# Kernel tuning notes

Measured on AMD Instinct MI355X. Metric: run time of the kernel, lower is better.

Reference implementation:

```python
import jax, jax.numpy as jnp
import numpy as np
import math

B, T, EMB = 4, 2048, 1024
PAD_TAIL = 256  # last keys marked as padding


def setup_inputs() -> dict:
    key = jax.random.key(0)
    kq, kk, kv = jax.random.split(key, 3)
    query = jax.random.normal(kq, (B, T, EMB), dtype=jnp.float32)
    k = jax.random.normal(kk, (B, T, EMB), dtype=jnp.float32)
    value = jax.random.normal(kv, (B, T, EMB), dtype=jnp.float32)
    # padding mask: 1 = valid, 0 = padded (last PAD_TAIL keys padded)
    attention_mask = jnp.concatenate(
        [jnp.ones((B, T - PAD_TAIL), dtype=jnp.int32),
         jnp.zeros((B, PAD_TAIL), dtype=jnp.int32)], axis=1)
    return {"query": query, "key": k, "value": value,
            "attention_mask": attention_mask}


def reference(query, key, value, attention_mask):
    Bq, Tq, emb = query.shape
    Tk = key.shape[1]
    scale = 1.0 / math.sqrt(emb)
    # [B, Tq, Tk]
    scores = jnp.einsum('bqd,bkd->bqk', query, key) * scale
    neg_inf = jnp.float32(-jnp.inf)
    if Tq == Tk:  # mask_future=True and square -> causal mask
        causal = jnp.triu(jnp.ones((Tq, Tk), dtype=bool), k=1)
        scores = jnp.where(causal[None, :, :], neg_inf, scores)
    key_pad = (attention_mask == 0)[:, None, :]  # [B, 1, Tk]
    scores = jnp.where(key_pad, neg_inf, scores)
    attn = jax.nn.softmax(scores, axis=-1)
    # attn_dropout = 0.0 -> identity
    out = jnp.einsum('bqk,bkd->bqd', attn, value)
    return out
```

## Files before the change

### kernel.cpp

```cpp
#include <hip/hip_runtime.h>
#include <stdint.h>

#define TB 2048
#define DD 1024

typedef __bf16 bf16x8 __attribute__((ext_vector_type(8)));
typedef float  f32x16 __attribute__((ext_vector_type(16)));
typedef int    int4v  __attribute__((ext_vector_type(4)));
typedef unsigned u32;

__device__ __forceinline__ u32 pack2(float hi, float lo) {
  return (__float_as_uint(hi) & 0xffff0000u) | (__float_as_uint(lo) >> 16);
}
__device__ __forceinline__ bf16x8 pack8(const float f[8]) {
  int4v w;
  w.x = (int)pack2(f[1], f[0]);
  w.y = (int)pack2(f[3], f[2]);
  w.z = (int)pack2(f[5], f[4]);
  w.w = (int)pack2(f[7], f[6]);
  return __builtin_bit_cast(bf16x8, w);
}

__global__ __launch_bounds__(256)
void conv_all(const float* __restrict__ Q, const float* __restrict__ K,
              const float* __restrict__ V,
              unsigned short* __restrict__ Qf, unsigned short* __restrict__ Kf,
              unsigned short* __restrict__ Vf) {
  __shared__ __align__(16) float t[64 * 260];
  if (blockIdx.x < 512) {
    const int isQ = blockIdx.x >> 8;
    const int bid = blockIdx.x & 255;
    const float* src0 = isQ ? Q : K;
    unsigned short* dst0 = isQ ? Qf : Kf;
    const float scl = isQ ? 0.03125f : 1.0f;
    const int b  = bid >> 6;
    const int kt = bid & 63;
    const int lt  = threadIdx.x & 63;
    const int row = lt & 31, hi = lt >> 5;
    const int wv  = threadIdx.x >> 6;
    const float* src = src0 + ((size_t)(b * TB + kt * 32 + row)) * DD + hi * 8;
    unsigned short* dst = dst0 + ((size_t)(b * 64 + kt) * 64) * 512 + lt * 8;
    #pragma unroll
    for (int i = 0; i < 16; ++i) {
      const int ds = wv + 4 * i;
      const float4 a = *(const float4*)(src + ds * 16);
      const float4 c = *(const float4*)(src + ds * 16 + 4);
      const float f[8] = {a.x*scl, a.y*scl, a.z*scl, a.w*scl,
                          c.x*scl, c.y*scl, c.z*scl, c.w*scl};
      *(int4v*)(dst + (size_t)ds * 512) = __builtin_bit_cast(int4v, pack8(f));
    }
  } else {
    const int bid = blockIdx.x - 512;
    const int b   = bid >> 7;
    const int kb  = (bid >> 2) & 31;
    const int db  = bid & 3;
    const int k0 = kb * 64, d0 = db * 256;
    {
      const int f = threadIdx.x & 63;
      const int r0 = threadIdx.x >> 6;
      #pragma unroll
      for (int i = 0; i < 16; ++i) {
        const int kloc = r0 + 4 * i;
        const float4 v4 = *(const float4*)(V + ((size_t)(b * TB + k0 + kloc)) * DD + d0 + f * 4);
        *(float4*)(t + kloc * 260 + f * 4) = v4;
      }
    }
    __syncthreads();
    const int lt  = threadIdx.x & 63;
    const int lo5 = lt & 31, hi = lt >> 5;
    const int kk  = threadIdx.x >> 6;
    #pragma unroll
    for (int dd = 0; dd < 8; ++dd) {
      float f[8];
      #pragma unroll
      for (int j = 0; j < 8; ++j)
        f[j] = t[(kk * 16 + hi * 8 + j) * 260 + dd * 32 + lo5];
      unsigned short* dst = Vf +
          (((size_t)(b * 32 + (d0 >> 5) + dd) * 128 + (k0 >> 4) + kk) * 64 + lt) * 8;
      *(int4v*)dst = __builtin_bit_cast(int4v, pack8(f));
    }
  }
}

__global__ __launch_bounds__(512, 2)
void fa_fwd_f32_v6(const unsigned short* __restrict__ Qf, const int* __restrict__ AM,
                   const unsigned short* __restrict__ Kf, const unsigned short* __restrict__ Vf,
                   unsigned short* __restrict__ OA, unsigned short* __restrict__ OB,
                   float* __restrict__ ML)
{
  __shared__ __align__(16) unsigned short lds_Q[64 * 64 * 8];
  __shared__ __align__(16) unsigned short lds_P[16 * 64 * 8];
  __shared__ float lds_red[8][32];
  __shared__ unsigned char lds_nib[512];
  __shared__ int lds_tvi;

  const int tid  = threadIdx.x;
  const int w    = tid >> 6;
  const int lane = tid & 63;
  const int lo5  = lane & 31;
  const int hi   = lane >> 5;

  const int bid  = blockIdx.x;
  const int xcd  = bid & 7, slot = bid >> 3;
  const int b    = xcd >> 1, x = xcd & 1;
  const int rank = slot >> 1, h = slot & 1;
  const int qt   = 63 - 2 * rank - x;
  const int q0   = qt << 5;

  {
    const char* qsrc = (const char*)Qf + ((size_t)(b * 64 + qt)) * 65536 + tid * 16;
    #pragma unroll
    for (int i = 0; i < 8; ++i)
      *(int4v*)((char*)lds_Q + tid * 16 + i * 8192) = *(const int4v*)(qsrc + (size_t)i * 8192);
  }
  if (tid == 0) lds_tvi = 0;
  __syncthreads();
  {
    const int4v mi = *(const int4v*)(AM + b * TB + 4 * tid);
    const unsigned char nib = (mi.x?1:0)|(mi.y?2:0)|(mi.z?4:0)|(mi.w?8:0);
    lds_nib[tid] = nib;
    if (nib) atomicOr(&lds_tvi, 1 << (tid >> 6));
  }
  __syncthreads();
  const int tvbits = lds_tvi;

  float m = -1e30f, l = 0.f;
  f32x16 oacc[4] = {f32x16{}, f32x16{}, f32x16{}, f32x16{}};

  const char* vb = (const char*)Vf + ((size_t)(b * 32 + 4 * w)) * 131072 + lane * 16;
  const int q = q0 + lo5;
  const int diag_kt = qt >> 3;

  const int nkt = diag_kt + 1;
  for (int kt = h; kt < nkt; kt += 2) {
    if (!(tvbits & (1 << kt))) continue;
    const int k0 = kt << 8;

    f32x16 s0{}, s1{};
    {
      const char* kp = (const char*)Kf + ((size_t)(b * 64 + kt * 8 + w)) * 65536 + lane * 16;
      const char* qp = (const char*)lds_Q + lane * 16;
      __builtin_amdgcn_s_setprio(1);
      #pragma unroll 4
      for (int ds = 0; ds < 64; ds += 2) {
        s0 = __builtin_amdgcn_mfma_f32_32x32x16_bf16(
            *(const bf16x8*)kp, *(const bf16x8*)qp, s0, 0, 0, 0);
        s1 = __builtin_amdgcn_mfma_f32_32x32x16_bf16(
            *(const bf16x8*)(kp + 1024), *(const bf16x8*)(qp + 1024), s1, 0, 0, 0);
        kp += 2048; qp += 2048;
      }
      __builtin_amdgcn_s_setprio(0);
    }

    u32 mw;
    {
      const u32* nw = (const u32*)(lds_nib + 64 * kt + 8 * w);
      const u32 n0 = nw[0], n1 = nw[1];
      mw = (n0 & 0xFu) | ((n0 >> 4) & 0xF0u) | ((n0 >> 8) & 0xF00u) | ((n0 >> 12) & 0xF000u);
      mw |= ((n1 & 0xFu) | ((n1 >> 4) & 0xF0u) | ((n1 >> 8) & 0xF00u) | ((n1 >> 12) & 0xF000u)) << 16;
    }
    float s[16];
    float mx = -1e30f;
    if (kt != diag_kt && mw == 0xffffffffu) {
      #pragma unroll
      for (int r = 0; r < 16; ++r) { s[r] = s0[r] + s1[r]; mx = fmaxf(mx, s[r]); }
    } else {
      #pragma unroll
      for (int r = 0; r < 16; ++r) {
        const int kl = (r & 3) + 8 * (r >> 2) + 4 * hi;
        const bool ok = (((mw >> kl) & 1u) != 0u) && (k0 + 32 * w + kl <= q);
        s[r] = ok ? (s0[r] + s1[r]) : -1e30f;
        mx = fmaxf(mx, s[r]);
      }
    }
    mx = fmaxf(mx, __shfl_xor(mx, 32, 64));
    if (lane < 32) lds_red[w][lo5] = mx;
    __syncthreads();

    float gm = m;
    #pragma unroll
    for (int j = 0; j < 8; ++j) gm = fmaxf(gm, lds_red[j][lo5]);
    const float sc = __expf(m - gm);
    m = gm;
    const float pm = fmaxf(gm, -1e28f);
    float ls = 0.f;
    #pragma unroll
    for (int r = 0; r < 16; ++r) { s[r] = __expf(s[r] - pm); ls += s[r]; }
    ls += __shfl_xor(ls, 32, 64);
    l = l * sc + ls;
    #pragma unroll
    for (int nb = 0; nb < 4; ++nb)
      #pragma unroll
      for (int r = 0; r < 16; ++r) oacc[nb][r] *= sc;

    {
      #pragma unroll
      for (int c = 0; c < 2; ++c) {
        const u32 pw0 = pack2(s[8*c+1], s[8*c+0]);
        const u32 pw1 = pack2(s[8*c+3], s[8*c+2]);
        const u32 pw2 = pack2(s[8*c+5], s[8*c+4]);
        const u32 pw3 = pack2(s[8*c+7], s[8*c+6]);
        const u32 px0 = (u32)__shfl_xor((int)pw0, 32, 64);
        const u32 px1 = (u32)__shfl_xor((int)pw1, 32, 64);
        const u32 px2 = (u32)__shfl_xor((int)pw2, 32, 64);
        const u32 px3 = (u32)__shfl_xor((int)pw3, 32, 64);
        int4v f;
        if (hi) { f.x=(int)px2; f.y=(int)px3; f.z=(int)pw2; f.w=(int)pw3; }
        else    { f.x=(int)pw0; f.y=(int)pw1; f.z=(int)px0; f.w=(int)px1; }
        *(int4v*)((char*)lds_P + ((2*w + c) * 64 + lane) * 16) = f;
      }
    }
    __syncthreads();

    __builtin_amdgcn_s_setprio(1);
    #pragma unroll 4
    for (int kcg = 0; kcg < 16; ++kcg) {
      const bf16x8 pb = *(const bf16x8*)((const char*)lds_P + (kcg * 64 + lane) * 16);
      const char* vp = vb + (size_t)(kt * 16 + kcg) * 1024;
      #pragma unroll
      for (int nb = 0; nb < 4; ++nb)
        oacc[nb] = __builtin_amdgcn_mfma_f32_32x32x16_bf16(
            *(const bf16x8*)(vp + (size_t)nb * 131072), pb, oacc[nb], 0, 0, 0);
    }
    __builtin_amdgcn_s_setprio(0);
  }

  {
    unsigned short* obase = (h ? OB : OA) + ((size_t)(b * TB + q0 + lo5)) * DD + 128 * w;
    #pragma unroll
    for (int nb = 0; nb < 4; ++nb) {
      #pragma unroll
      for (int m2 = 0; m2 < 4; ++m2) {
        const u32 e0 = pack2(oacc[nb][4*m2+1], oacc[nb][4*m2+0]);
        const u32 e1 = pack2(oacc[nb][4*m2+3], oacc[nb][4*m2+2]);
        const u32 y0 = (u32)__shfl_xor((int)e0, 32, 64);
        const u32 y1 = (u32)__shfl_xor((int)e1, 32, 64);
        if (hi == (nb >> 1)) {
          int4v f;
          if (hi) { f.x=(int)y0; f.y=(int)y1; f.z=(int)e0; f.w=(int)e1; }
          else    { f.x=(int)e0; f.y=(int)e1; f.z=(int)y0; f.w=(int)y1; }
          *(int4v*)(obase + 32 * nb + 8 * m2) = f;
        }
      }
    }
  }
  if (lane < 32) lds_red[w][lo5] = l;
  __syncthreads();
  if (w == 0 && lane < 32) {
    float lt = 0.f;
    #pragma unroll
    for (int j = 0; j < 8; ++j) lt += lds_red[j][lo5];
    const int row = b * TB + q0 + lo5;
    ML[h * 16384 + row] = m;
    ML[h * 16384 + 8192 + row] = lt;
  }
}

__global__ __launch_bounds__(256)
void merge_v4(float* __restrict__ O, const unsigned short* __restrict__ OA,
              const unsigned short* __restrict__ OB, const float* __restrict__ ML) {
  const int idx = blockIdx.x * 256 + threadIdx.x;
  const int row = idx >> 6;
  const float mAv = ML[row],         lAv = ML[8192 + row];
  const float mBv = ML[16384 + row], lBv = ML[24576 + row];
  const float m = fmaxf(mAv, mBv);
  const float eA = __expf(mAv - m), eB = __expf(mBv - m);
  const float inv = 1.0f / (eA * lAv + eB * lBv);
  const float fa = eA * inv, fb = eB * inv;
  const uint4* pa = (const uint4*)(OA + (size_t)idx * 16);
  const uint4* pb = (const uint4*)(OB + (size_t)idx * 16);
  float4* od = (float4*)(O + (size_t)idx * 16);
  #pragma unroll
  for (int g = 0; g < 2; ++g) {
    const uint4 ua = pa[g], ub = pb[g];
    const u32 wa[4] = {ua.x, ua.y, ua.z, ua.w};
    const u32 wb[4] = {ub.x, ub.y, ub.z, ub.w};
    float out[8];
    #pragma unroll
    for (int i = 0; i < 4; ++i) {
      const float aLo = __uint_as_float(wa[i] << 16);
      const float aHi = __uint_as_float(wa[i] & 0xffff0000u);
      const float bLo = __uint_as_float(wb[i] << 16);
      const float bHi = __uint_as_float(wb[i] & 0xffff0000u);
      out[2*i]   = fa * aLo + fb * bLo;
      out[2*i+1] = fa * aHi + fb * bHi;
    }
    od[2*g]   = make_float4(out[0], out[1], out[2], out[3]);
    od[2*g+1] = make_float4(out[4], out[5], out[6], out[7]);
  }
}

__global__ __launch_bounds__(512, 2)
void fa_fwd_f32_v1(const float* __restrict__ Q, const float* __restrict__ K,
                   const float* __restrict__ V, const int* __restrict__ AM,
                   float* __restrict__ O)
{
  __shared__ __align__(16) float lds_part[8][32 * 68];
  __shared__ __align__(16) unsigned short lds_Pf[32][72];
  __shared__ float lds_m[32], lds_l[32], lds_scale[32];
  __shared__ unsigned lds_mask32[TB / 4];
  __shared__ int lds_tv[32];

  const int tid  = threadIdx.x;
  const int w    = tid >> 6;
  const int lane = tid & 63;
  const int lo5  = lane & 31;
  const int hi   = lane >> 5;

  const int bid  = blockIdx.x;
  const int xcd  = bid & 7;
  const int slot = bid >> 3;
  const int b    = xcd >> 1;
  const int half = xcd & 1;
  const int qt   = half ? (16 + slot) : (slot < 16 ? slot : 32 + slot);
  const int q0   = qt << 5;

  const int4v mi = *(const int4v*)(AM + b * TB + 4 * tid);
  const unsigned mw = (mi.x ? 1u : 0u) | (mi.y ? 0x100u : 0u) |
                      (mi.z ? 0x10000u : 0u) | (mi.w ? 0x1000000u : 0u);
  lds_mask32[tid] = mw;
  if (tid < 32) { lds_tv[tid] = 0; lds_m[tid] = -1e30f; lds_l[tid] = 0.0f; }
  __syncthreads();
  if (mw) lds_tv[tid >> 4] = 1;

  bf16x8 qf[8];
  {
    const float* qrow = Q + ((size_t)b * TB + q0 + lo5) * DD + w * 128 + hi * 8;
    #pragma unroll
    for (int kk = 0; kk < 8; ++kk) {
      const float4 a = *(const float4*)(qrow + kk * 16);
      const float4 c = *(const float4*)(qrow + kk * 16 + 4);
      const float f[8] = {a.x * 0.03125f, a.y * 0.03125f, a.z * 0.03125f, a.w * 0.03125f,
                          c.x * 0.03125f, c.y * 0.03125f, c.z * 0.03125f, c.w * 0.03125f};
      qf[kk] = pack8(f);
    }
  }

  f32x16 oacc[4] = {f32x16{}, f32x16{}, f32x16{}, f32x16{}};
  const float* kbat = K + (size_t)b * TB * DD + w * 128 + hi * 8;
  const float* vbat = V + (size_t)b * TB * DD + w * 128;
  __syncthreads();

  const int nkt = (qt >> 1) + 1;
  for (int kt = 0; kt < nkt; ++kt) {
    if (!lds_tv[kt]) continue;
    const int k0 = kt << 6;
    f32x16 s0{}, s1{};
    const float* kb0 = kbat + (size_t)(k0 + lo5) * DD;
    #pragma unroll
    for (int kk = 0; kk < 8; ++kk) {
      const float4 a0 = *(const float4*)(kb0 + kk * 16);
      const float4 a1 = *(const float4*)(kb0 + kk * 16 + 4);
      const float f0[8] = {a0.x, a0.y, a0.z, a0.w, a1.x, a1.y, a1.z, a1.w};
      s0 = __builtin_amdgcn_mfma_f32_32x32x16_bf16(qf[kk], pack8(f0), s0, 0, 0, 0);
      const float4 c0 = *(const float4*)(kb0 + (size_t)32 * DD + kk * 16);
      const float4 c1 = *(const float4*)(kb0 + (size_t)32 * DD + kk * 16 + 4);
      const float f1[8] = {c0.x, c0.y, c0.z, c0.w, c1.x, c1.y, c1.z, c1.w};
      s1 = __builtin_amdgcn_mfma_f32_32x32x16_bf16(qf[kk], pack8(f1), s1, 0, 0, 0);
    }
    {
      float* wp = lds_part[w];
      const int pos = lo5 + (hi << 5);
      #pragma unroll
      for (int r = 0; r < 16; ++r) {
        wp[r * 68 + pos]        = s0[r];
        wp[(16 + r) * 68 + pos] = s1[r];
      }
    }
    __syncthreads();
    {
      const int r = tid >> 4, g = tid & 15;
      const int regp  = (r & 3) | (((r >> 3) & 3) << 2);
      const int plane = ((g >> 3) << 4) + regp;
      const int pos   = ((4 * g) & 31) + (((r >> 2) & 1) << 5);
      float s[4] = {0.f, 0.f, 0.f, 0.f};
      #pragma unroll
      for (int ww = 0; ww < 8; ++ww) {
        const float4 v4 = *(const float4*)&lds_part[ww][plane * 68 + pos];
        s[0] += v4.x; s[1] += v4.y; s[2] += v4.z; s[3] += v4.w;
      }
      const unsigned mv = lds_mask32[(k0 >> 2) + g];
      const int qq = q0 + r;
      #pragma unroll
      for (int i = 0; i < 4; ++i) {
        const int kg = k0 + 4 * g + i;
        const bool ok = (((mv >> (8 * i)) & 0xffu) != 0u) && (kg <= qq);
        if (!ok) s[i] = -1e30f;
      }
      float mx = fmaxf(fmaxf(s[0], s[1]), fmaxf(s[2], s[3]));
      #pragma unroll
      for (int d = 1; d < 16; d <<= 1) mx = fmaxf(mx, __shfl_xor(mx, d, 64));
      const float mold = lds_m[r];
      const float mnew = fmaxf(mold, mx);
      float p[4], lsv = 0.f;
      #pragma unroll
      for (int i = 0; i < 4; ++i) { p[i] = __expf(s[i] - mnew); lsv += p[i]; }
      #pragma unroll
      for (int d = 1; d < 16; d <<= 1) lsv += __shfl_xor(lsv, d, 64);
      const float resc = __expf(mold - mnew);
      if (g == 0) {
        lds_m[r]     = mnew;
        lds_l[r]     = lds_l[r] * resc + lsv;
        lds_scale[r] = resc;
      }
      unsigned* pp = (unsigned*)&lds_Pf[r][4 * g];
      pp[0] = pack2(p[1], p[0]);
      pp[1] = pack2(p[3], p[2]);
    }
    __syncthreads();
    {
      float scv[16];
      #pragma unroll
      for (int reg = 0; reg < 16; ++reg)
        scv[reg] = lds_scale[(reg & 3) + ((reg >> 2) << 3) + (hi << 2)];
      #pragma unroll
      for (int nb = 0; nb < 4; ++nb) {
        #pragma unroll
        for (int reg = 0; reg < 16; ++reg) oacc[nb][reg] *= scv[reg];
      }
      bf16x8 pf[4];
      #pragma unroll
      for (int kc = 0; kc < 4; ++kc)
        pf[kc] = __builtin_bit_cast(bf16x8, *(const int4v*)&lds_Pf[lo5][kc * 16 + hi * 8]);
      const float* vbp = vbat + (size_t)k0 * DD + lo5;
      #pragma unroll
      for (int kc = 0; kc < 4; ++kc) {
        const float* vr = vbp + (size_t)(kc * 16 + hi * 8) * DD;
        float fv[4][8];
        #pragma unroll
        for (int j = 0; j < 8; ++j) {
          const float* vrj = vr + (size_t)j * DD;
          #pragma unroll
          for (int nb = 0; nb < 4; ++nb) fv[nb][j] = vrj[nb * 32];
        }
        #pragma unroll
        for (int nb = 0; nb < 4; ++nb)
          oacc[nb] = __builtin_amdgcn_mfma_f32_32x32x16_bf16(pf[kc], pack8(fv[nb]), oacc[nb], 0, 0, 0);
      }
    }
    __syncthreads();
  }

  float il[16];
  #pragma unroll
  for (int reg = 0; reg < 16; ++reg)
    il[reg] = 1.0f / lds_l[(reg & 3) + ((reg >> 2) << 3) + (hi << 2)];
  float* ob = O + ((size_t)b * TB + q0) * DD + w * 128;
  #pragma unroll
  for (int nb = 0; nb < 4; ++nb) {
    #pragma unroll
    for (int reg = 0; reg < 16; ++reg) {
      const int row = (reg & 3) + ((reg >> 2) << 3) + (hi << 2);
      ob[(size_t)row * DD + nb * 32 + lo5] = oacc[nb][reg] * il[reg];
    }
  }
}

extern "C" void kernel_launch(void* const* d_in, const int* in_sizes, int n_in,
                              void* d_out, int out_size, void* d_ws, size_t ws_size,
                              hipStream_t stream) {
  const float* Q  = (const float*)d_in[0];
  const float* K  = (const float*)d_in[1];
  const float* V  = (const float*)d_in[2];
  const int*   AM = (const int*)d_in[3];
  float* O = (float*)d_out;
  (void)in_sizes; (void)n_in; (void)out_size;

  const size_t SZ = 16777216;
  const size_t need = 5 * SZ + 131072;
  if (ws_size >= need) {
    unsigned short* Kf = (unsigned short*)d_ws;
    unsigned short* Vf = (unsigned short*)((char*)d_ws + SZ);
    unsigned short* Qf = (unsigned short*)((char*)d_ws + 2 * SZ);
    unsigned short* OA = (unsigned short*)((char*)d_ws + 3 * SZ);
    unsigned short* OB = (unsigned short*)((char*)d_ws + 4 * SZ);
    float*          ML = (float*)((char*)d_ws + 5 * SZ);
    hipLaunchKernelGGL(conv_all, dim3(1024), dim3(256), 0, stream, Q, K, V, Qf, Kf, Vf);
    hipLaunchKernelGGL(fa_fwd_f32_v6, dim3(512), dim3(512), 0, stream,
                       Qf, AM, Kf, Vf, OA, OB, ML);
    hipLaunchKernelGGL(merge_v4, dim3(2048), dim3(256), 0, stream, O, OA, OB, ML);
  } else {
    hipLaunchKernelGGL(fa_fwd_f32_v1, dim3(256), dim3(512), 0, stream, Q, K, V, AM, O);
  }
}
```

Baseline: 144.9 us.

## Software-pipeline K and V global loads into register ring buffers with explicit vmcnt waits

Replaces direct global-memory MFMA operand loads with inline-asm global_load_dwordx4 into 16-entry register ring buffers for K and V. Loads are issued two groups ahead and gated with s_waitcnt vmcnt, so memory latency overlaps the MFMAs. V loads for the tile are issued before the softmax so they arrive during the reduction. The __syncthreads calls are swapped for a custom LDS-only barrier. This costs many more VGPRs under launch_bounds(512,2), which risks spills, and the hand-written waitcnt logic could be wrong if the compiler issues other vector memory operations.

```diff
diff --git a/kernel.cpp b/kernel.cpp
--- a/kernel.cpp
+++ b/kernel.cpp
@@ -82,8 +82,15 @@
   }
 }
 
+__device__ __forceinline__ void lds_barrier() {
+  __builtin_amdgcn_sched_barrier(0);
+  asm volatile("s_waitcnt lgkmcnt(0)");
+  __builtin_amdgcn_s_barrier();
+  __builtin_amdgcn_sched_barrier(0);
+}
+
 __global__ __launch_bounds__(512, 2)
-void fa_fwd_f32_v6(const unsigned short* __restrict__ Qf, const int* __restrict__ AM,
+void fa_fwd_f32_v9(const unsigned short* __restrict__ Qf, const int* __restrict__ AM,
                    const unsigned short* __restrict__ Kf, const unsigned short* __restrict__ Vf,
                    unsigned short* __restrict__ OA, unsigned short* __restrict__ OB,
                    float* __restrict__ ML)
@@ -140,16 +147,47 @@
     {
       const char* kp = (const char*)Kf + ((size_t)(b * 64 + kt * 8 + w)) * 65536 + lane * 16;
       const char* qp = (const char*)lds_Q + lane * 16;
+      int4v kb[16];
+      #pragma unroll
+      for (int i = 0; i < 16; ++i)
+        asm volatile("global_load_dwordx4 %0, %1, off"
+                     : "=v"(kb[i]) : "v"(kp + (size_t)i * 1024));
       __builtin_amdgcn_s_setprio(1);
-      #pragma unroll 4
-      for (int ds = 0; ds < 64; ds += 2) {
-        s0 = __builtin_amdgcn_mfma_f32_32x32x16_bf16(
-            *(const bf16x8*)kp, *(const bf16x8*)qp, s0, 0, 0, 0);
-        s1 = __builtin_amdgcn_mfma_f32_32x32x16_bf16(
-            *(const bf16x8*)(kp + 1024), *(const bf16x8*)(qp + 1024), s1, 0, 0, 0);
-        kp += 2048; qp += 2048;
+      #pragma unroll
+      for (int g = 0; g < 8; ++g) {
+        if (g < 7) asm volatile("s_waitcnt vmcnt(8)");
+        else       asm volatile("s_waitcnt vmcnt(0)");
+        __builtin_amdgcn_sched_barrier(0);
+        #pragma unroll
+        for (int j = 0; j < 8; j += 2) {
+          const int ds = 8 * g + j;
+          s0 = __builtin_amdgcn_mfma_f32_32x32x16_bf16(
+              __builtin_bit_cast(bf16x8, kb[ds & 15]),
+              *(const bf16x8*)(qp + (size_t)ds * 1024), s0, 0, 0, 0);
+          s1 = __builtin_amdgcn_mfma_f32_32x32x16_bf16(
+              __builtin_bit_cast(bf16x8, kb[(ds + 1) & 15]),
+              *(const bf16x8*)(qp + (size_t)(ds + 1) * 1024), s1, 0, 0, 0);
+        }
+        if (g < 6) {
+          #pragma unroll
+          for (int j = 0; j < 8; ++j) {
+            const int dsn = 8 * (g + 2) + j;
+            asm volatile("global_load_dwordx4 %0, %1, off"
+                         : "=v"(kb[dsn & 15]) : "v"(kp + (size_t)dsn * 1024));
+          }
+        }
       }
       __builtin_amdgcn_s_setprio(0);
+    }
+
+    int4v vbv[16];
+    {
+      const char* vt = vb + (size_t)kt * 16384;
+      #pragma unroll
+      for (int i = 0; i < 16; ++i)
+        asm volatile("global_load_dwordx4 %0, %1, off"
+                     : "=v"(vbv[i])
+                     : "v"(vt + (size_t)(i >> 2) * 1024 + (size_t)(i & 3) * 131072));
     }
 
     u32 mw;
@@ -175,7 +213,7 @@
     }
     mx = fmaxf(mx, __shfl_xor(mx, 32, 64));
     if (lane < 32) lds_red[w][lo5] = mx;
-    __syncthreads();
+    lds_barrier();
 
     float gm = m;
     #pragma unroll
@@ -210,19 +248,39 @@
         *(int4v*)((char*)lds_P + ((2*w + c) * 64 + lane) * 16) = f;
       }
     }
-    __syncthreads();
-
-    __builtin_amdgcn_s_setprio(1);
-    #pragma unroll 4
-    for (int kcg = 0; kcg < 16; ++kcg) {
-      const bf16x8 pb = *(const bf16x8*)((const char*)lds_P + (kcg * 64 + lane) * 16);
-      const char* vp = vb + (size_t)(kt * 16 + kcg) * 1024;
-      #pragma unroll
-      for (int nb = 0; nb < 4; ++nb)
-        oacc[nb] = __builtin_amdgcn_mfma_f32_32x32x16_bf16(
-            *(const bf16x8*)(vp + (size_t)nb * 131072), pb, oacc[nb], 0, 0, 0);
-    }
-    __builtin_amdgcn_s_setprio(0);
+    lds_barrier();
+
+    {
+      const char* vt = vb + (size_t)kt * 16384;
+      __builtin_amdgcn_s_setprio(1);
+      #pragma unroll
+      for (int g = 0; g < 8; ++g) {
+        if (g < 7) asm volatile("s_waitcnt vmcnt(8)");
+        else       asm volatile("s_waitcnt vmcnt(0)");
+        __builtin_amdgcn_sched_barrier(0);
+        #pragma unroll
+        for (int kk = 0; kk < 2; ++kk) {
+          const int kcg = 2 * g + kk;
+          const bf16x8 pb = *(const bf16x8*)((const char*)lds_P + (kcg * 64 + lane) * 16);
+          #pragma unroll
+          for (int nb = 0; nb < 4; ++nb) {
+            const int idx = kcg * 4 + nb;
+            oacc[nb] = __builtin_amdgcn_mfma_f32_32x32x16_bf16(
+                __builtin_bit_cast(bf16x8, vbv[idx & 15]), pb, oacc[nb], 0, 0, 0);
+          }
+        }
+        if (g < 6) {
+          #pragma unroll
+          for (int j = 0; j < 8; ++j) {
+            const int idxn = 8 * (g + 2) + j;
+            asm volatile("global_load_dwordx4 %0, %1, off"
+                         : "=v"(vbv[idxn & 15])
+                         : "v"(vt + (size_t)(idxn >> 2) * 1024 + (size_t)(idxn & 3) * 131072));
+          }
+        }
+      }
+      __builtin_amdgcn_s_setprio(0);
+    }
   }
 
   {
@@ -476,7 +534,7 @@
     unsigned short* OB = (unsigned short*)((char*)d_ws + 4 * SZ);
     float*          ML = (float*)((char*)d_ws + 5 * SZ);
     hipLaunchKernelGGL(conv_all, dim3(1024), dim3(256), 0, stream, Q, K, V, Qf, Kf, Vf);
-    hipLaunchKernelGGL(fa_fwd_f32_v6, dim3(512), dim3(512), 0, stream,
+    hipLaunchKernelGGL(fa_fwd_f32_v9, dim3(512), dim3(512), 0, stream,
                        Qf, AM, Kf, Vf, OA, OB, ML);
     hipLaunchKernelGGL(merge_v4, dim3(2048), dim3(256), 0, stream, O, OA, OB, ML);
   } else {
```

Measured after the change: 117.7 us. 1.23x faster.
